# Kernel optimization log

Hardware: AMD Instinct MI355X
Metric: run time of the kernel (lower is better)

## Reference

```python
import jax, jax.numpy as jnp
import numpy as np

N_NODES = 50000
N_EDGES = 600000
D_FEAT = 128
OUT_DIM = 128


def setup_inputs() -> dict:
    key = jax.random.key(0)
    k1, k2, k3, k4 = jax.random.split(key, 4)
    self_feat = jax.random.normal(k1, (N_NODES, D_FEAT), dtype=jnp.float32)
    nbr_feat = jax.random.normal(k2, (N_EDGES, D_FEAT), dtype=jnp.float32)
    relation_src_indices = jax.random.randint(k3, (N_EDGES,), 0, N_NODES, dtype=jnp.int32)
    # Dense(output_dim, use_bias=False), input dim = 2*D_FEAT due to concat
    W = jax.random.normal(k4, (2 * D_FEAT, OUT_DIM), dtype=jnp.float32) * (1.0 / np.sqrt(2 * D_FEAT))
    return {"self_feat": self_feat, "nbr_feat": nbr_feat,
            "relation_src_indices": relation_src_indices, "W": W}


def reference(self_feat, nbr_feat, relation_src_indices, W):
    num_nodes = self_feat.shape[0]
    # unsorted_segment_mean: sum / count, 0 for empty segments (TF semantics)
    seg_sum = jax.ops.segment_sum(nbr_feat, relation_src_indices, num_segments=num_nodes)
    counts = jax.ops.segment_sum(jnp.ones((nbr_feat.shape[0],), dtype=nbr_feat.dtype),
                                 relation_src_indices, num_segments=num_nodes)
    agg = jnp.where(counts[:, None] > 0, seg_sum / jnp.maximum(counts[:, None], 1.0), 0.0)
    out = jnp.concatenate([self_feat, agg], axis=-1)  # [N, 2*D]
    return out @ W  # [N, OUT_DIM]
```

## Files before the change

### kernel.cpp

```cpp
#include <hip/hip_runtime.h>

#define D 128
#define K2 256

typedef float vfloat4 __attribute__((ext_vector_type(4)));


__global__ void hist_kernel(const int* __restrict__ idx, int* __restrict__ cnt, int n) {
    int e = blockIdx.x * 256 + threadIdx.x;
    if (e < n) atomicAdd(&cnt[idx[e]], 1);
}

__global__ void reduce_kernel(const int* __restrict__ cnt, int* __restrict__ bsum, int n) {
    __shared__ int s[256];
    int i = blockIdx.x * 256 + threadIdx.x;
    s[threadIdx.x] = (i < n) ? cnt[i] : 0;
    __syncthreads();
    for (int d = 128; d > 0; d >>= 1) {
        if (threadIdx.x < d) s[threadIdx.x] += s[threadIdx.x + d];
        __syncthreads();
    }
    if (threadIdx.x == 0) bsum[blockIdx.x] = s[0];
}

__global__ void scan_bsum_kernel(int* __restrict__ bsum, int* __restrict__ off, int nb, int n) {
    __shared__ int s[256];
    int v = (threadIdx.x < nb) ? bsum[threadIdx.x] : 0;
    s[threadIdx.x] = v;
    __syncthreads();
    for (int d = 1; d < 256; d <<= 1) {
        int t = (threadIdx.x >= d) ? s[threadIdx.x - d] : 0;
        __syncthreads();
        s[threadIdx.x] += t;
        __syncthreads();
    }
    if (threadIdx.x < nb) bsum[threadIdx.x] = s[threadIdx.x] - v;
    if (threadIdx.x == 255) off[n] = s[255];
}

__global__ void scan_kernel(const int* __restrict__ cnt, const int* __restrict__ bsum,
                            int* __restrict__ off, int* __restrict__ cur, int n) {
    __shared__ int s[256];
    int i = blockIdx.x * 256 + threadIdx.x;
    int v = (i < n) ? cnt[i] : 0;
    s[threadIdx.x] = v;
    __syncthreads();
    for (int d = 1; d < 256; d <<= 1) {
        int t = (threadIdx.x >= d) ? s[threadIdx.x - d] : 0;
        __syncthreads();
        s[threadIdx.x] += t;
        __syncthreads();
    }
    if (i < n) {
        int e = bsum[blockIdx.x] + s[threadIdx.x] - v;
        off[i] = e;
        cur[i] = e;
    }
}

__global__ void scatter_kernel(const int* __restrict__ idx, int* __restrict__ cur,
                               int* __restrict__ eid, int n) {
    int e = blockIdx.x * 256 + threadIdx.x;
    if (e < n) {
        int p = atomicAdd(&cur[idx[e]], 1);
        eid[p] = e;
    }
}


__global__ __launch_bounds__(64) void aggregate_kernel(const float* __restrict__ nbr,
                                                       const int* __restrict__ eid,
                                                       const int* __restrict__ off,
                                                       float* __restrict__ agg) {
    const int node = blockIdx.x;
    const int beg = off[node], end = off[node + 1];
    const int t = threadIdx.x;
    const int h = t >> 5;
    const int l = t & 31;
    const vfloat4* __restrict__ rows = (const vfloat4*)nbr;
    vfloat4 acc = {0.f, 0.f, 0.f, 0.f};
    int j = beg;
    for (; j + 8 <= end; j += 8) {
        int e0 = eid[j + 0 + h];
        int e1 = eid[j + 2 + h];
        int e2 = eid[j + 4 + h];
        int e3 = eid[j + 6 + h];
        vfloat4 v0 = __builtin_nontemporal_load(rows + (size_t)e0 * 32 + l);
        vfloat4 v1 = __builtin_nontemporal_load(rows + (size_t)e1 * 32 + l);
        vfloat4 v2 = __builtin_nontemporal_load(rows + (size_t)e2 * 32 + l);
        vfloat4 v3 = __builtin_nontemporal_load(rows + (size_t)e3 * 32 + l);
        acc += (v0 + v1) + (v2 + v3);
    }
    if (j + 4 <= end) {
        int e0 = eid[j + 0 + h];
        int e1 = eid[j + 2 + h];
        vfloat4 v0 = __builtin_nontemporal_load(rows + (size_t)e0 * 32 + l);
        vfloat4 v1 = __builtin_nontemporal_load(rows + (size_t)e1 * 32 + l);
        acc += v0 + v1;
        j += 4;
    }
    for (; j < end; j += 2) {
        int jj = j + h;
        if (jj < end) {
            int e = eid[jj];
            vfloat4 v = __builtin_nontemporal_load(rows + (size_t)e * 32 + l);
            acc += v;
        }
    }
    acc.x += __shfl_xor(acc.x, 32);
    acc.y += __shfl_xor(acc.y, 32);
    acc.z += __shfl_xor(acc.z, 32);
    acc.w += __shfl_xor(acc.w, 32);
    int c = end - beg;
    float inv = (c > 0) ? 1.0f / (float)c : 0.0f;
    if (h == 0) {
        vfloat4 o = acc * inv;
        *((vfloat4*)agg + (size_t)node * 32 + l) = o;
    }
}


#define MT 64
#define KB 32
#define XP (MT + 4)

__global__ __launch_bounds__(128) void matmul_kernel(const float* __restrict__ self,
                                                     const float* __restrict__ agg,
                                                     const float* __restrict__ W,
                                                     float* __restrict__ out, int nNodes) {
    __shared__ float Xs[KB][XP];
    __shared__ float Ws[KB][D];
    const int t = threadIdx.x;
    const int m_base = blockIdx.x * MT;
    const int n0 = (t & 15) * 8;
    const int m0 = (t >> 4) * 8;

    float acc[8][8];
#pragma unroll
    for (int i = 0; i < 8; ++i)
#pragma unroll
        for (int j = 0; j < 8; ++j) acc[i][j] = 0.f;

    for (int k0 = 0; k0 < K2; k0 += KB) {
        const float* src = (k0 < D) ? self : agg;
        const int koff = k0 & (D - 1);
#pragma unroll
        for (int it = 0; it < 4; ++it) {
            int lin = t + it * 128;
            int row = lin >> 3;
            int k4 = lin & 7;
            int gr = m_base + row;
            if (gr >= nNodes) gr = nNodes - 1;
            float4 v = *(const float4*)(src + (size_t)gr * D + koff + k4 * 4);
            Xs[k4 * 4 + 0][row] = v.x;
            Xs[k4 * 4 + 1][row] = v.y;
            Xs[k4 * 4 + 2][row] = v.z;
            Xs[k4 * 4 + 3][row] = v.w;
        }
#pragma unroll
        for (int it = 0; it < 8; ++it) {
            int lin = t + it * 128;
            int kk = lin >> 5;
            int n4 = lin & 31;
            *(float4*)(&Ws[kk][n4 * 4]) = *(const float4*)(W + (size_t)(k0 + kk) * D + n4 * 4);
        }
        __syncthreads();

#pragma unroll
        for (int kk4 = 0; kk4 < KB / 4; ++kk4) {
            float4 xa[4], xb[4], wa[4], wb[4];
#pragma unroll
            for (int kq = 0; kq < 4; ++kq) {
                int k = kk4 * 4 + kq;
                xa[kq] = *(const float4*)(&Xs[k][m0]);
                xb[kq] = *(const float4*)(&Xs[k][m0 + 4]);
                wa[kq] = *(const float4*)(&Ws[k][n0]);
                wb[kq] = *(const float4*)(&Ws[k][n0 + 4]);
            }
#pragma unroll
            for (int kq = 0; kq < 4; ++kq) {
                const float xr[8] = {xa[kq].x, xa[kq].y, xa[kq].z, xa[kq].w,
                                     xb[kq].x, xb[kq].y, xb[kq].z, xb[kq].w};
                const float wr[8] = {wa[kq].x, wa[kq].y, wa[kq].z, wa[kq].w,
                                     wb[kq].x, wb[kq].y, wb[kq].z, wb[kq].w};
#pragma unroll
                for (int i = 0; i < 8; ++i)
#pragma unroll
                    for (int j = 0; j < 8; ++j) acc[i][j] += xr[i] * wr[j];
            }
        }
        __syncthreads();
    }

#pragma unroll
    for (int i = 0; i < 8; ++i) {
        int gr = m_base + m0 + i;
        if (gr < nNodes) {
            float4 o0 = make_float4(acc[i][0], acc[i][1], acc[i][2], acc[i][3]);
            float4 o1 = make_float4(acc[i][4], acc[i][5], acc[i][6], acc[i][7]);
            *(float4*)(out + (size_t)gr * D + n0) = o0;
            *(float4*)(out + (size_t)gr * D + n0 + 4) = o1;
        }
    }
}


extern "C" void kernel_launch(void* const* d_in, const int* in_sizes, int n_in,
                              void* d_out, int out_size, void* d_ws, size_t ws_size,
                              hipStream_t stream) {
    const float* self = (const float*)d_in[0];
    const float* nbr = (const float*)d_in[1];
    const int* idx = (const int*)d_in[2];
    const float* W = (const float*)d_in[3];
    float* out = (float*)d_out;

    const int nNodes = in_sizes[0] / D;
    const int nEdges = in_sizes[2];
    const int nb = (nNodes + 255) / 256;

    int* cnt = (int*)d_ws;
    int* off = cnt + nNodes;
    int* cur = off + (nNodes + 1);
    int* bsum = cur + nNodes;
    int* eid = bsum + 256;

    hipMemsetAsync(cnt, 0, (size_t)nNodes * sizeof(int), stream);
    hist_kernel<<<(nEdges + 255) / 256, 256, 0, stream>>>(idx, cnt, nEdges);
    reduce_kernel<<<nb, 256, 0, stream>>>(cnt, bsum, nNodes);
    scan_bsum_kernel<<<1, 256, 0, stream>>>(bsum, off, nb, nNodes);
    scan_kernel<<<nb, 256, 0, stream>>>(cnt, bsum, off, cur, nNodes);
    scatter_kernel<<<(nEdges + 255) / 256, 256, 0, stream>>>(idx, cur, eid, nEdges);

    aggregate_kernel<<<nNodes, 64, 0, stream>>>(nbr, eid, off, out);
    matmul_kernel<<<(nNodes + MT - 1) / MT, 128, 0, stream>>>(self, out, W, out, nNodes);
}
```

Measured before the change: 531.8 us.

## Merge three-pass prefix scan into one block, deepen gather unroll, nontemporal output stores

Replaces the reduce, block-sum scan and final scan kernels with a single 1024-thread block that serially sums contiguous chunks, scans the partials in shared memory, then writes offsets. This removes two kernel launches and the bsum workspace. The aggregate loop now issues 16 edge rows per iteration for more loads in flight, and the matmul writes its output with nontemporal stores. The single-block scan puts about 50 sequential, uncoalesced reads per thread on one CU, which could cost more than the launches it saves.

```diff
diff --git a/kernel.cpp b/kernel.cpp
--- a/kernel.cpp
+++ b/kernel.cpp
@@ -11,51 +11,34 @@
     if (e < n) atomicAdd(&cnt[idx[e]], 1);
 }
 
-__global__ void reduce_kernel(const int* __restrict__ cnt, int* __restrict__ bsum, int n) {
-    __shared__ int s[256];
-    int i = blockIdx.x * 256 + threadIdx.x;
-    s[threadIdx.x] = (i < n) ? cnt[i] : 0;
+__global__ __launch_bounds__(1024) void scan_all_kernel(const int* __restrict__ cnt,
+                                                        int* __restrict__ off,
+                                                        int* __restrict__ cur, int n) {
+    __shared__ int s[1024];
+    const int t = threadIdx.x;
+    const int chunk = (n + 1023) / 1024;
+    int b = t * chunk;
+    int e = b + chunk;
+    if (b > n) b = n;
+    if (e > n) e = n;
+    int sum = 0;
+    for (int i = b; i < e; ++i) sum += cnt[i];
+    s[t] = sum;
     __syncthreads();
-    for (int d = 128; d > 0; d >>= 1) {
-        if (threadIdx.x < d) s[threadIdx.x] += s[threadIdx.x + d];
-        __syncthreads();
-    }
-    if (threadIdx.x == 0) bsum[blockIdx.x] = s[0];
-}
-
-__global__ void scan_bsum_kernel(int* __restrict__ bsum, int* __restrict__ off, int nb, int n) {
-    __shared__ int s[256];
-    int v = (threadIdx.x < nb) ? bsum[threadIdx.x] : 0;
-    s[threadIdx.x] = v;
-    __syncthreads();
-    for (int d = 1; d < 256; d <<= 1) {
-        int t = (threadIdx.x >= d) ? s[threadIdx.x - d] : 0;
-        __syncthreads();
-        s[threadIdx.x] += t;
-        __syncthreads();
-    }
-    if (threadIdx.x < nb) bsum[threadIdx.x] = s[threadIdx.x] - v;
-    if (threadIdx.x == 255) off[n] = s[255];
-}
-
-__global__ void scan_kernel(const int* __restrict__ cnt, const int* __restrict__ bsum,
-                            int* __restrict__ off, int* __restrict__ cur, int n) {
-    __shared__ int s[256];
-    int i = blockIdx.x * 256 + threadIdx.x;
-    int v = (i < n) ? cnt[i] : 0;
-    s[threadIdx.x] = v;
-    __syncthreads();
-    for (int d = 1; d < 256; d <<= 1) {
-        int t = (threadIdx.x >= d) ? s[threadIdx.x - d] : 0;
-        __syncthreads();
-        s[threadIdx.x] += t;
-        __syncthreads();
-    }
-    if (i < n) {
-        int e = bsum[blockIdx.x] + s[threadIdx.x] - v;
-        off[i] = e;
-        cur[i] = e;
-    }
+    int v = sum;
+    for (int d = 1; d < 1024; d <<= 1) {
+        int u = (t >= d) ? s[t - d] : 0;
+        __syncthreads();
+        s[t] += u;
+        __syncthreads();
+    }
+    int run = s[t] - v;
+    for (int i = b; i < e; ++i) {
+        off[i] = run;
+        cur[i] = run;
+        run += cnt[i];
+    }
+    if (t == 1023) off[n] = s[1023];
 }
 
 __global__ void scatter_kernel(const int* __restrict__ idx, int* __restrict__ cur,
@@ -80,20 +63,30 @@
     const vfloat4* __restrict__ rows = (const vfloat4*)nbr;
     vfloat4 acc = {0.f, 0.f, 0.f, 0.f};
     int j = beg;
-    for (; j + 8 <= end; j += 8) {
-        int e0 = eid[j + 0 + h];
-        int e1 = eid[j + 2 + h];
-        int e2 = eid[j + 4 + h];
-        int e3 = eid[j + 6 + h];
+    for (; j + 16 <= end; j += 16) {
+        int e0 = eid[j + 0 + h], e1 = eid[j + 2 + h], e2 = eid[j + 4 + h], e3 = eid[j + 6 + h];
+        int e4 = eid[j + 8 + h], e5 = eid[j + 10 + h], e6 = eid[j + 12 + h], e7 = eid[j + 14 + h];
+        vfloat4 v0 = __builtin_nontemporal_load(rows + (size_t)e0 * 32 + l);
+        vfloat4 v1 = __builtin_nontemporal_load(rows + (size_t)e1 * 32 + l);
+        vfloat4 v2 = __builtin_nontemporal_load(rows + (size_t)e2 * 32 + l);
+        vfloat4 v3 = __builtin_nontemporal_load(rows + (size_t)e3 * 32 + l);
+        vfloat4 v4 = __builtin_nontemporal_load(rows + (size_t)e4 * 32 + l);
+        vfloat4 v5 = __builtin_nontemporal_load(rows + (size_t)e5 * 32 + l);
+        vfloat4 v6 = __builtin_nontemporal_load(rows + (size_t)e6 * 32 + l);
+        vfloat4 v7 = __builtin_nontemporal_load(rows + (size_t)e7 * 32 + l);
+        acc += ((v0 + v1) + (v2 + v3)) + ((v4 + v5) + (v6 + v7));
+    }
+    if (j + 8 <= end) {
+        int e0 = eid[j + 0 + h], e1 = eid[j + 2 + h], e2 = eid[j + 4 + h], e3 = eid[j + 6 + h];
         vfloat4 v0 = __builtin_nontemporal_load(rows + (size_t)e0 * 32 + l);
         vfloat4 v1 = __builtin_nontemporal_load(rows + (size_t)e1 * 32 + l);
         vfloat4 v2 = __builtin_nontemporal_load(rows + (size_t)e2 * 32 + l);
         vfloat4 v3 = __builtin_nontemporal_load(rows + (size_t)e3 * 32 + l);
         acc += (v0 + v1) + (v2 + v3);
+        j += 8;
     }
     if (j + 4 <= end) {
-        int e0 = eid[j + 0 + h];
-        int e1 = eid[j + 2 + h];
+        int e0 = eid[j + 0 + h], e1 = eid[j + 2 + h];
         vfloat4 v0 = __builtin_nontemporal_load(rows + (size_t)e0 * 32 + l);
         vfloat4 v1 = __builtin_nontemporal_load(rows + (size_t)e1 * 32 + l);
         acc += v0 + v1;
@@ -103,8 +96,7 @@
         int jj = j + h;
         if (jj < end) {
             int e = eid[jj];
-            vfloat4 v = __builtin_nontemporal_load(rows + (size_t)e * 32 + l);
-            acc += v;
+            acc += __builtin_nontemporal_load(rows + (size_t)e * 32 + l);
         }
     }
     acc.x += __shfl_xor(acc.x, 32);
@@ -196,10 +188,10 @@
     for (int i = 0; i < 8; ++i) {
         int gr = m_base + m0 + i;
         if (gr < nNodes) {
-            float4 o0 = make_float4(acc[i][0], acc[i][1], acc[i][2], acc[i][3]);
-            float4 o1 = make_float4(acc[i][4], acc[i][5], acc[i][6], acc[i][7]);
-            *(float4*)(out + (size_t)gr * D + n0) = o0;
-            *(float4*)(out + (size_t)gr * D + n0 + 4) = o1;
+            vfloat4 o0 = {acc[i][0], acc[i][1], acc[i][2], acc[i][3]};
+            vfloat4 o1 = {acc[i][4], acc[i][5], acc[i][6], acc[i][7]};
+            __builtin_nontemporal_store(o0, (vfloat4*)(out + (size_t)gr * D + n0));
+            __builtin_nontemporal_store(o1, (vfloat4*)(out + (size_t)gr * D + n0 + 4));
         }
     }
 }
@@ -216,19 +208,15 @@
 
     const int nNodes = in_sizes[0] / D;
     const int nEdges = in_sizes[2];
-    const int nb = (nNodes + 255) / 256;
 
     int* cnt = (int*)d_ws;
     int* off = cnt + nNodes;
     int* cur = off + (nNodes + 1);
-    int* bsum = cur + nNodes;
-    int* eid = bsum + 256;
-
-    hipMemsetAsync(cnt, 0, (size_t)nNodes * sizeof(int), stream);
+    int* eid = cur + nNodes;
+
+    (void)hipMemsetAsync(cnt, 0, (size_t)nNodes * sizeof(int), stream);
     hist_kernel<<<(nEdges + 255) / 256, 256, 0, stream>>>(idx, cnt, nEdges);
-    reduce_kernel<<<nb, 256, 0, stream>>>(cnt, bsum, nNodes);
-    scan_bsum_kernel<<<1, 256, 0, stream>>>(bsum, off, nb, nNodes);
-    scan_kernel<<<nb, 256, 0, stream>>>(cnt, bsum, off, cur, nNodes);
+    scan_all_kernel<<<1, 1024, 0, stream>>>(cnt, off, cur, nNodes);
     scatter_kernel<<<(nEdges + 255) / 256, 256, 0, stream>>>(idx, cur, eid, nEdges);
 
     aggregate_kernel<<<nNodes, 64, 0, stream>>>(nbr, eid, off, out);
```

Measured after the change: 630.7 us. 1.19x slower.
